# Performance work log

Measured on AMD Instinct MI355X. Metric: run time of the kernel, lower is better.

Reference implementation:

```python
import jax, jax.numpy as jnp
import numpy as np
import math

B, L, D = 2, 4096, 1024
H, DK, DV = 4, 256, 256
CHUNK = 32
PROB_FLOOR = 0.02


def _l2norm(x, eps=1e-6):
    return x * jax.lax.rsqrt(jnp.sum(x * x, -1, keepdims=True) + eps)


def _silu(x):
    return x * jax.nn.sigmoid(x)


def _short_conv(x, w):
    # x: (b, l, c); w: (c, K). Depthwise causal conv + SiLU (ShortConvolution).
    K = w.shape[-1]
    xp = jnp.pad(x, ((0, 0), (K - 1, 0), (0, 0)))
    y = sum(xp[:, j:j + x.shape[1], :] * w[:, j] for j in range(K))
    return _silu(y)


def _fir_conv(x, filt):
    # x: (b, l, h, d); filt: (h, d, K). Depthwise causal FIR, no activation.
    b, l, h, d = x.shape
    K = filt.shape[-1]
    xf = jnp.pad(x.reshape(b, l, h * d).transpose(0, 2, 1), ((0, 0), (0, 0), (K - 1, 0)))
    w = filt.reshape(h * d, 1, K)
    y = jax.lax.conv_general_dilated(xf, w, (1,), 'VALID',
                                     dimension_numbers=('NCH', 'OIH', 'NCH'),
                                     feature_group_count=h * d)
    return y.transpose(0, 2, 1).reshape(b, l, h, d)


def _delta_rule_chunkwise(q, k, v, beta, chunk=CHUNK):
    # q,k: (b,h,L,dk); v: (b,h,L,dv); beta: (b,h,L). L % chunk == 0.
    b, h, Lq, dk = q.shape
    dv = v.shape[-1]
    n = Lq // chunk
    q = _l2norm(q)
    k = _l2norm(k)
    v = v * beta[..., None]
    kb = k * beta[..., None]
    rs = lambda t: t.reshape(b, h, n, chunk, t.shape[-1])
    qc, kc, vc, kbc = rs(q), rs(k), rs(v), rs(kb)
    strict_lower = jnp.tril(jnp.ones((chunk, chunk), bool), -1)
    # M = strictly-lower part of k_beta @ k^T; the in-place row recursion in the
    # torch code computes (I + M)^{-1} (unit lower-triangular inverse).
    M = jnp.where(strict_lower, jnp.einsum('bhncd,bhnmd->bhncm', kbc, kc), 0.0)
    eye = jnp.eye(chunk, dtype=q.dtype)
    T = jax.scipy.linalg.solve_triangular(eye + M, jnp.broadcast_to(eye, M.shape),
                                          lower=True, unit_diagonal=True)
    u = T @ vc       # (b,h,n,c,dv)
    w = T @ kbc      # (b,h,n,c,dk)
    incl_lower = jnp.tril(jnp.ones((chunk, chunk), bool), 0)

    def step(S, xs):
        q_i, k_i, u_i, w_i = xs  # (b,h,c,d)
        attn = jnp.where(incl_lower, q_i @ k_i.swapaxes(-1, -2), 0.0)
        u_adj = u_i - w_i @ S
        out_i = q_i @ S + attn @ u_adj
        S = S + k_i.swapaxes(-1, -2) @ u_adj
        return S, out_i

    S0 = jnp.zeros((b, h, dk, dv), q.dtype)
    xs = tuple(jnp.moveaxis(t, 2, 0) for t in (qc, kc, u, w))
    S, out = jax.lax.scan(step, S0, xs)
    out = jnp.moveaxis(out, 0, 2).reshape(b, h, Lq, dv)
    return out, S


def _rmsnorm(x, w, eps=1e-5):
    return x * jax.lax.rsqrt(jnp.mean(x * x, -1, keepdims=True) + eps) * w


def _per_head_stats(x):
    mean = jnp.mean(x, -1, keepdims=True)
    var = jnp.var(x, -1, keepdims=True)
    am = jnp.mean(jnp.abs(x), -1, keepdims=True)
    l2 = jnp.sqrt(jnp.sum(x * x, -1, keepdims=True))
    return jnp.concatenate([mean, var, am, l2], -1)  # (...,4)


def setup_inputs() -> dict:
    key = jax.random.key(0)
    ks = jax.random.split(key, 16)
    s = 0.02
    hidden_gate = D * 2 // 2  # fusion_hidden_mult=2 -> 1024
    gate_in_dim = D + 16
    inp = {
        'hidden_states': jax.random.normal(ks[0], (B, L, D), jnp.float32),
        'q_w': jax.random.normal(ks[1], (D, D), jnp.float32) * s,
        'k_w': jax.random.normal(ks[2], (D, D), jnp.float32) * s,
        'v_w': jax.random.normal(ks[3], (D, D), jnp.float32) * s,
        'b_w': jax.random.normal(ks[4], (H, D), jnp.float32) * s,
        'q_cw': jax.random.normal(ks[5], (D, 4), jnp.float32) * s,
        'k_cw': jax.random.normal(ks[6], (D, 4), jnp.float32) * s,
        'v_cw': jax.random.normal(ks[7], (D, 4), jnp.float32) * s,
        'fir_short_w': jax.random.normal(ks[8], (H, DV, 5), jnp.float32) * s,
        'fir_long_w': jax.random.normal(ks[9], (H, DV, 64), jnp.float32) * s,
        'mlp1_w': jax.random.normal(ks[10], (hidden_gate, gate_in_dim), jnp.float32) * s,
        'mlp1_b': jnp.zeros((hidden_gate,), jnp.float32),
        'mlp2_w': jax.random.normal(ks[11], (4, hidden_gate), jnp.float32) * s,
        'mlp2_b': jnp.array([-0.5, -0.5, 1.0, 3.0], jnp.float32),
        'logit_temp': jnp.full((1,), math.log(math.expm1(0.7)), jnp.float32),
        'conv_res_logit': jnp.full((H,), -2.0, jnp.float32),
        'norm_w': jnp.ones((DV,), jnp.float32),
        'o_w': jax.random.normal(ks[12], (D, D), jnp.float32) * s,
    }
    return inp


def _forward(hidden_states, q_w, k_w, v_w, b_w, q_cw, k_cw, v_cw,
             fir_short_w, fir_long_w, mlp1_w, mlp1_b, mlp2_w, mlp2_b,
             logit_temp, conv_res_logit, norm_w, o_w):
    b, l, _ = hidden_states.shape
    # projections + short causal depthwise convs (SiLU, qk_activation='silu')
    q_in = _short_conv(hidden_states @ q_w.T, q_cw)
    k_in = _short_conv(hidden_states @ k_w.T, k_cw)
    v_in = _short_conv(hidden_states @ v_w.T, v_cw)
    q = q_in.reshape(b, l, H, DK)
    k = k_in.reshape(b, l, H, DK)
    v_direct = v_in.reshape(b, l, H, DV)
    # qk_activation='silu' handled in conv; qk_norm='l2' handled inside delta rule
    beta = jnp.maximum(jax.nn.sigmoid(hidden_states @ b_w.T), 1e-6)  # (b,l,H)
    delta_out, _S = _delta_rule_chunkwise(
        q.transpose(0, 2, 1, 3), k.transpose(0, 2, 1, 3),
        v_direct.transpose(0, 2, 1, 3), beta.transpose(0, 2, 1))
    delta_out = delta_out.transpose(0, 2, 1, 3)  # (b,l,H,DV)
    local_short = _fir_conv(v_direct, fir_short_w)
    local_long = _fir_conv(v_direct, fir_long_w)
    stats = jnp.concatenate([_per_head_stats(local_short), _per_head_stats(local_long),
                             _per_head_stats(delta_out), _per_head_stats(v_direct)], -1)  # (b,l,H,16)
    hs_exp = jnp.broadcast_to(hidden_states[:, :, None, :], (b, l, H, hidden_states.shape[-1]))
    gate_in = jnp.concatenate([hs_exp, stats], -1)  # (b,l,H,D+16)
    h1 = jax.nn.gelu(gate_in @ mlp1_w.T + mlp1_b)
    logits = h1 @ mlp2_w.T + mlp2_b  # (b,l,H,4)
    temp = jax.nn.softplus(logit_temp)
    p = jax.nn.softmax(logits / temp, -1)
    p = jnp.maximum(p, PROB_FLOOR)
    p = p / jnp.sum(p, -1, keepdims=True)
    o = (p[..., 0:1] * local_short + p[..., 1:2] * local_long +
         p[..., 2:3] * delta_out + p[..., 3:4] * v_direct)
    # balanced residual conv injection (per-head learned static gate)
    o = o + jax.nn.sigmoid(conv_res_logit)[None, None, :, None] * local_short
    o = _rmsnorm(o, norm_w)
    o = o.reshape(b, l, H * DV) @ o_w.T
    return o


def reference(hidden_states, q_w, k_w, v_w, b_w, q_cw, k_cw, v_cw,
              fir_short_w, fir_long_w, mlp1_w, mlp1_b, mlp2_w, mlp2_b,
              logit_temp, conv_res_logit, norm_w, o_w):
    return _forward(hidden_states, q_w, k_w, v_w, b_w, q_cw, k_cw, v_cw,
                    fir_short_w, fir_long_w, mlp1_w, mlp1_b, mlp2_w, mlp2_b,
                    logit_temp, conv_res_logit, norm_w, o_w)
```

## Files before the change

### kernel.cpp

```cpp
#include <hip/hip_runtime.h>
#include <hip/hip_bf16.h>
#include <math.h>

#define NB 2
#define NL 4096
#define ND 1024
#define NH 4
#define NDK 256
#define NDV 256
#define NCH 128
#define NBL (NB*NL)

typedef __attribute__((ext_vector_type(8))) short short8;
typedef __attribute__((ext_vector_type(4))) short short4v;
typedef __attribute__((ext_vector_type(4))) float float4v;

#define MFMA16(a,b,c) __builtin_amdgcn_mfma_f32_16x16x32_bf16(a,b,c,0,0,0)

__device__ __forceinline__ short f2bs(float f){
  union { __hip_bfloat16 h; short s; } u; u.h = __float2bfloat16(f); return u.s;
}
__device__ __forceinline__ float bs2f(short s){
  union { float f; unsigned u; } u; u.u = ((unsigned)(unsigned short)s) << 16; return u.f;
}
__device__ __forceinline__ void store_c(float* p, float v){ *p = v; }
__device__ __forceinline__ void store_c(short* p, float v){ *p = f2bs(v); }

__device__ __forceinline__ void gload16(const short* g, short* l){
  __builtin_amdgcn_global_load_lds(
      (const __attribute__((address_space(1))) unsigned int*)g,
      (__attribute__((address_space(3))) unsigned int*)l, 16, 0, 0);
}
__device__ __forceinline__ void lds_barrier(){
  asm volatile("s_waitcnt lgkmcnt(0)" ::: "memory");
  __builtin_amdgcn_s_barrier();
  asm volatile("" ::: "memory");
}

__global__ void k_cast8(const float* __restrict__ s, short* __restrict__ d, int n8){
  int i = blockIdx.x*256 + threadIdx.x;
  if(i >= n8) return;
  const float4v a = *(const float4v*)(s + (size_t)i*8);
  const float4v b = *(const float4v*)(s + (size_t)i*8 + 4);
  short8 o;
  #pragma unroll
  for(int j=0;j<4;j++){ o[j] = f2bs(a[j]); o[4+j] = f2bs(b[j]); }
  *(short8*)(d + (size_t)i*8) = o;
}
__global__ void k_cast_w1a(const float* __restrict__ s, short* __restrict__ d){
  int i = blockIdx.x*256 + threadIdx.x;
  int r = i >> 7, c0 = (i & 127)*8;
  const float* sp = s + (size_t)r*1040 + c0;
  const float4v a = *(const float4v*)sp;
  const float4v b = *(const float4v*)(sp + 4);
  short8 o;
  #pragma unroll
  for(int j=0;j<4;j++){ o[j] = f2bs(a[j]); o[4+j] = f2bs(b[j]); }
  *(short8*)(d + (size_t)r*1024 + c0) = o;
}

__launch_bounds__(256)
__global__ void k_gemm4(const short* __restrict__ A, const short* __restrict__ Bt,
                        short* __restrict__ oq, short* __restrict__ ok,
                        short* __restrict__ ov, short* __restrict__ og){
  const int K = 1024;
  __shared__ short As[128*32];
  __shared__ short Bs[128*32];
  const int tid = threadIdx.x;
  const int w = tid >> 6, lane = tid & 63, lr = lane & 15, lg = lane >> 4;
  const int bm = blockIdx.x*128 + (w >> 1)*64;
  const int bnl = (blockIdx.y & 7)*128 + (w & 1)*64;
  short* C = (blockIdx.y>>3)==0 ? oq : (blockIdx.y>>3)==1 ? ok
           : (blockIdx.y>>3)==2 ? ov : og;
  float4v acc[4][4];
  #pragma unroll
  for(int i=0;i<4;i++)
    #pragma unroll
    for(int j=0;j<4;j++) acc[i][j] = (float4v){0.f,0.f,0.f,0.f};
  const short* ga0 = A  + (size_t)(blockIdx.x*128 + (tid>>2))*K + (tid&3)*8;
  const short* ga1 = ga0 + (size_t)64*K;
  const short* gb0 = Bt + (size_t)(blockIdx.y*128 + (tid>>2))*K + (tid&3)*8;
  const short* gb1 = gb0 + (size_t)64*K;
  short* la0 = As + w*512;
  short* la1 = As + 2048 + w*512;
  short* lb0 = Bs + w*512;
  short* lb1 = Bs + 2048 + w*512;
  const int arow = (w>>1)*64, brow = (w&1)*64;
  for(int kk=0; kk<K; kk+=32){
    gload16(ga0+kk, la0);
    gload16(ga1+kk, la1);
    gload16(gb0+kk, lb0);
    gload16(gb1+kk, lb1);
    __syncthreads();
    short8 a[4], b[4];
    #pragma unroll
    for(int i=0;i<4;i++) a[i] = *(const short8*)(As + (arow + i*16 + lr)*32 + lg*8);
    #pragma unroll
    for(int j=0;j<4;j++) b[j] = *(const short8*)(Bs + (brow + j*16 + lr)*32 + lg*8);
    #pragma unroll
    for(int i=0;i<4;i++)
      #pragma unroll
      for(int j=0;j<4;j++)
        acc[i][j] = MFMA16(a[i], b[j], acc[i][j]);
    __syncthreads();
  }
  #pragma unroll
  for(int i=0;i<4;i++){
    int row0 = bm + i*16 + lg*4;
    #pragma unroll
    for(int j=0;j<4;j++){
      short* cp = C + (size_t)row0*1024 + bnl + j*16 + lr;
      #pragma unroll
      for(int r=0;r<4;r++) cp[(size_t)r*1024] = f2bs(acc[i][j][r]);
    }
  }
}

template<typename OT>
__launch_bounds__(256)
__global__ void k_gemm(const short* __restrict__ A, const short* __restrict__ Bt,
                       OT* __restrict__ C, int M, int N, int K){
  __shared__ short As[128*32];
  __shared__ short Bs[128*32];
  const int tid = threadIdx.x;
  const int w = tid >> 6, lane = tid & 63, lr = lane & 15, lg = lane >> 4;
  const int bm = blockIdx.x*128 + (w >> 1)*64;
  const int bn = blockIdx.y*128 + (w & 1)*64;
  float4v acc[4][4];
  #pragma unroll
  for(int i=0;i<4;i++)
    #pragma unroll
    for(int j=0;j<4;j++) acc[i][j] = (float4v){0.f,0.f,0.f,0.f};
  const short* ga0 = A  + (size_t)(blockIdx.x*128 + (tid>>2))*K + (tid&3)*8;
  const short* ga1 = ga0 + (size_t)64*K;
  const short* gb0 = Bt + (size_t)(blockIdx.y*128 + (tid>>2))*K + (tid&3)*8;
  const short* gb1 = gb0 + (size_t)64*K;
  short* la0 = As + w*512;
  short* la1 = As + 2048 + w*512;
  short* lb0 = Bs + w*512;
  short* lb1 = Bs + 2048 + w*512;
  const int arow = (w>>1)*64, brow = (w&1)*64;
  for(int kk=0; kk<K; kk+=32){
    gload16(ga0+kk, la0);
    gload16(ga1+kk, la1);
    gload16(gb0+kk, lb0);
    gload16(gb1+kk, lb1);
    __syncthreads();
    short8 a[4], b[4];
    #pragma unroll
    for(int i=0;i<4;i++) a[i] = *(const short8*)(As + (arow + i*16 + lr)*32 + lg*8);
    #pragma unroll
    for(int j=0;j<4;j++) b[j] = *(const short8*)(Bs + (brow + j*16 + lr)*32 + lg*8);
    #pragma unroll
    for(int i=0;i<4;i++)
      #pragma unroll
      for(int j=0;j<4;j++)
        acc[i][j] = MFMA16(a[i], b[j], acc[i][j]);
    __syncthreads();
  }
  #pragma unroll
  for(int i=0;i<4;i++){
    int row0 = bm + i*16 + lg*4;
    #pragma unroll
    for(int j=0;j<4;j++){
      OT* cp = C + (size_t)row0*N + bn + j*16 + lr;
      #pragma unroll
      for(int r=0;r<4;r++) store_c(cp + (size_t)r*N, acc[i][j][r]);
    }
  }
}

__global__ void k_conv_silu(const short* __restrict__ x, const float* __restrict__ wgt,
                            short* __restrict__ y){
  int i8 = blockIdx.x*256 + threadIdx.x;
  int c0 = (i8 & 127)*8;
  int l = (i8 >> 7) & (NL-1);
  size_t base = (size_t)i8*8;
  short8 xv[4];
  #pragma unroll
  for(int t=0;t<4;t++)
    xv[t] = (l >= t) ? *(const short8*)(x + base - (size_t)t*1024)
                     : (short8){0,0,0,0,0,0,0,0};
  short8 o;
  #pragma unroll
  for(int j=0;j<8;j++){
    const float4v w4 = *(const float4v*)(wgt + (c0+j)*4);
    float acc = 0.f;
    #pragma unroll
    for(int t=0;t<4;t++) if(l >= t) acc += bs2f(xv[t][j]) * w4[3-t];
    o[j] = f2bs(acc / (1.f + __expf(-acc)));
  }
  *(short8*)(y + base) = o;
}

__global__ void k_beta(const float* __restrict__ hs, const float* __restrict__ bw,
                       float* __restrict__ beta){
  int w = threadIdx.x >> 6, lane = threadIdx.x & 63;
  int bl = blockIdx.x*4 + w;
  const float* x = hs + (size_t)bl*1024;
  float a[4] = {0.f,0.f,0.f,0.f};
  for(int d=lane; d<1024; d+=64){
    float xv = x[d];
    #pragma unroll
    for(int hh=0;hh<4;hh++) a[hh] += xv * bw[hh*1024 + d];
  }
  #pragma unroll
  for(int off=32; off; off>>=1)
    #pragma unroll
    for(int hh=0;hh<4;hh++) a[hh] += __shfl_down(a[hh], off);
  if(lane == 0)
    #pragma unroll
    for(int hh=0;hh<4;hh++)
      beta[(size_t)bl*4 + hh] = fmaxf(1.f/(1.f+__expf(-a[hh])), 1e-6f);
}

#define PADA 260
__launch_bounds__(256)
__global__ void k_phaseA(const short* __restrict__ q, const short* __restrict__ k,
                         const short* __restrict__ v, const float* __restrict__ beta,
                         short* __restrict__ qn_o, short* __restrict__ wn_o,
                         short* __restrict__ kT_o, short* __restrict__ at_o,
                         float* __restrict__ u_o){
  __shared__ float qn[32*PADA];
  __shared__ float kn[32*PADA];
  __shared__ float vb[32*PADA];
  __shared__ float kb[32*PADA];
  __shared__ float Ml[32*33];
  __shared__ float bet[32];
  const int tid = threadIdx.x;
  const int n = blockIdx.x % NCH;
  const int h = (blockIdx.x / NCH) % NH;
  const int b = blockIdx.x / (NCH*NH);
  size_t rowbase = ((size_t)b*NL + n*32)*1024 + h*256;
  if(tid < 32) bet[tid] = beta[((size_t)b*NL + n*32 + tid)*4 + h];
  for(int r=0;r<32;r++){
    qn[r*PADA + tid] = bs2f(q[rowbase + (size_t)r*1024 + tid]);
    kn[r*PADA + tid] = bs2f(k[rowbase + (size_t)r*1024 + tid]);
    vb[r*PADA + tid] = bs2f(v[rowbase + (size_t)r*1024 + tid]);
  }
  __syncthreads();
  {
    int row = tid >> 3, sub = tid & 7;
    float sq = 0.f, sk = 0.f;
    for(int kk=0; kk<32; kk++){
      int d = sub + 8*kk;
      float a0 = qn[row*PADA+d]; sq += a0*a0;
      float a1 = kn[row*PADA+d]; sk += a1*a1;
    }
    #pragma unroll
    for(int off=1; off<8; off<<=1){ sq += __shfl_xor(sq, off); sk += __shfl_xor(sk, off); }
    float rq = rsqrtf(sq + 1e-6f), rk = rsqrtf(sk + 1e-6f);
    float be = bet[row];
    for(int kk=0; kk<32; kk++){
      int d = sub + 8*kk;
      qn[row*PADA+d] *= rq;
      float kv = kn[row*PADA+d]*rk;
      kn[row*PADA+d] = kv;
      kb[row*PADA+d] = kv*be;
      vb[row*PADA+d] *= be;
    }
  }
  __syncthreads();
  {
    int w = tid >> 6, lane = tid & 63, lr = lane & 15, lg = lane >> 4;
    int m0 = (w & 1)*16;
    const float* Asrc = (w < 2) ? kb : qn;
    float4v acc0 = (float4v){0.f,0.f,0.f,0.f}, acc1 = (float4v){0.f,0.f,0.f,0.f};
    for(int kc=0; kc<8; kc++){
      int kof = kc*32 + lg*8;
      short8 af, b0, b1;
      const float* ap  = Asrc + (m0+lr)*PADA + kof;
      const float* bp0 = kn + lr*PADA + kof;
      const float* bp1 = kn + (16+lr)*PADA + kof;
      #pragma unroll
      for(int j=0;j<8;j++){ af[j]=f2bs(ap[j]); b0[j]=f2bs(bp0[j]); b1[j]=f2bs(bp1[j]); }
      acc0 = MFMA16(af, b0, acc0);
      acc1 = MFMA16(af, b1, acc1);
    }
    if(w < 2){
      #pragma unroll
      for(int r=0;r<4;r++){
        int row = m0 + lg*4 + r;
        Ml[row*33 + lr]      = (lr      < row) ? acc0[r] : 0.f;
        Ml[row*33 + 16 + lr] = ((16+lr) < row) ? acc1[r] : 0.f;
      }
    } else {
      size_t abase = (size_t)blockIdx.x * 1024;
      #pragma unroll
      for(int r=0;r<4;r++){
        int row = m0 + lg*4 + r;
        at_o[abase + row*32 + lr]      = (lr      <= row) ? f2bs(acc0[r]) : (short)0;
        at_o[abase + row*32 + 16 + lr] = ((16+lr) <= row) ? f2bs(acc1[r]) : (short)0;
      }
    }
  }
  __syncthreads();
  {
    int d = tid;
    for(int i=1;i<32;i++){
      float su = 0.f, sw = 0.f;
      const float* Mr = Ml + i*33;
      for(int t=0;t<i;t++){
        float m = Mr[t];
        su += m * vb[t*PADA + d];
        sw += m * kb[t*PADA + d];
      }
      vb[i*PADA + d] -= su;
      kb[i*PADA + d] -= sw;
    }
  }
  __syncthreads();
  {
    size_t obase = (size_t)blockIdx.x * 8192;
    for(int it=0; it<32; it++){
      int idx = it*256 + tid;
      qn_o[obase + idx] = f2bs(qn[it*PADA + tid]);
      wn_o[obase + idx] = f2bs(-kb[it*PADA + tid]);
      u_o [obase + idx] = vb[it*PADA + tid];
      int tt = idx & 31, dd = idx >> 5;
      kT_o[obase + idx] = f2bs(kn[tt*PADA + dd]);
    }
  }
}

struct FragsB {
  short8 a[8];
  short8 kt[4];
  short8 at;
  float4v u;
};

__device__ __forceinline__ void loadFrags(FragsB& f, size_t cb,
    const short* __restrict__ qn, const short* __restrict__ wn,
    const short* __restrict__ kT, const short* __restrict__ at,
    const float* __restrict__ u, int w, int lr, int lg, int m0, int c0){
  const short* kT_b = kT + cb*8192;
  #pragma unroll
  for(int mi=0;mi<4;mi++)
    f.kt[mi] = *(const short8*)(kT_b + ((w*4+mi)*16 + lr)*32 + lg*8);
  if(w < 2){
    const short* wn_b = wn + cb*8192;
    #pragma unroll
    for(int kc=0;kc<8;kc++)
      f.a[kc] = *(const short8*)(wn_b + (m0+lr)*256 + kc*32 + lg*8);
    const float* up = u + cb*8192 + (size_t)(m0 + lg*4)*256 + c0 + lr;
    #pragma unroll
    for(int r=0;r<4;r++) f.u[r] = up[(size_t)r*256];
  } else {
    const short* qn_b = qn + cb*8192;
    #pragma unroll
    for(int kc=0;kc<8;kc++)
      f.a[kc] = *(const short8*)(qn_b + (m0+lr)*256 + kc*32 + lg*8);
    f.at = *(const short8*)(at + cb*1024 + (m0+lr)*32 + lg*8);
  }
}

__device__ __forceinline__ void computeChunk(const FragsB& f, int n,
    float4v (&Sreg)[4], float* __restrict__ ua, short* __restrict__ ScT,
    short* __restrict__ dout, int b, int h, int c0,
    int w, int lr, int lg, int m0, int swz){
  char* scb = (char*)ScT;
  lds_barrier();
  float4v oacc = (float4v){0.f,0.f,0.f,0.f};
  if(w < 2){
    float4v acc = f.u, acc2 = (float4v){0.f,0.f,0.f,0.f};
    #pragma unroll
    for(int kc=0;kc<4;kc++){
      short8 s0 = *(const short8*)(scb + (((lr<<9) + ((kc*32 + lg*8)<<1)) ^ swz));
      short8 s1 = *(const short8*)(scb + (((lr<<9) + (((kc+4)*32 + lg*8)<<1)) ^ swz));
      acc  = MFMA16(f.a[kc],   s0, acc);
      acc2 = MFMA16(f.a[kc+4], s1, acc2);
    }
    #pragma unroll
    for(int r=0;r<4;r++) ua[(m0 + lg*4 + r)*18 + lr] = acc[r] + acc2[r];
  } else {
    float4v acc2 = (float4v){0.f,0.f,0.f,0.f};
    #pragma unroll
    for(int kc=0;kc<4;kc++){
      short8 s0 = *(const short8*)(scb + (((lr<<9) + ((kc*32 + lg*8)<<1)) ^ swz));
      short8 s1 = *(const short8*)(scb + (((lr<<9) + (((kc+4)*32 + lg*8)<<1)) ^ swz));
      oacc = MFMA16(f.a[kc],   s0, oacc);
      acc2 = MFMA16(f.a[kc+4], s1, acc2);
    }
    #pragma unroll
    for(int r=0;r<4;r++) oacc[r] += acc2[r];
  }
  lds_barrier();
  short8 bu;
  #pragma unroll
  for(int j=0;j<8;j++) bu[j] = f2bs(ua[(lg*8 + j)*18 + lr]);
  if(w >= 2){
    oacc = MFMA16(f.at, bu, oacc);
    short* ob = dout + ((size_t)b*NL + n*32 + m0 + lg*4)*1024 + h*256 + c0 + lr;
    #pragma unroll
    for(int r=0;r<4;r++) ob[(size_t)r*1024] = f2bs(oacc[r]);
  }
  #pragma unroll
  for(int mi=0; mi<4; mi++){
    Sreg[mi] = MFMA16(f.kt[mi], bu, Sreg[mi]);
    int rowb = (w*4 + mi)*16 + lg*4;
    short4v pk;
    #pragma unroll
    for(int r=0;r<4;r++) pk[r] = f2bs(Sreg[mi][r]);
    *(short4v*)(scb + (((lr<<9) + (rowb<<1)) ^ swz)) = pk;
  }
}

__launch_bounds__(256, 1)
__global__ void k_phaseB(const short* __restrict__ qn, const short* __restrict__ wn,
                         const short* __restrict__ kT, const short* __restrict__ at,
                         const float* __restrict__ u, short* __restrict__ dout){
  __shared__ float ua[32*18];
  __shared__ short ScT[4096];
  const int tid = threadIdx.x;
  const int chain = blockIdx.x & 7;
  const int cblk = blockIdx.x >> 3;
  const int b = chain >> 2, h = chain & 3;
  const int c0 = cblk * 16;
  for(int i=tid; i<4096; i+=256) ScT[i] = 0;
  const int w = tid >> 6, lane = tid & 63, lr = lane & 15, lg = lane >> 4;
  const int m0 = (w & 1)*16;
  const size_t chunkbase = (size_t)(b*NH + h) * NCH;
  const int swz = (lr & 7) << 4;
  float4v Sreg[4];
  #pragma unroll
  for(int mi=0;mi<4;mi++) Sreg[mi] = (float4v){0.f,0.f,0.f,0.f};
  __syncthreads();
  FragsB fA, fB;
  loadFrags(fA, chunkbase, qn, wn, kT, at, u, w, lr, lg, m0, c0);
  for(int n=0; n<NCH; n+=2){
    loadFrags(fB, chunkbase + n+1, qn, wn, kT, at, u, w, lr, lg, m0, c0);
    computeChunk(fA, n, Sreg, ua, ScT, dout, b, h, c0, w, lr, lg, m0, swz);
    if(n+2 < NCH)
      loadFrags(fA, chunkbase + n+2, qn, wn, kT, at, u, w, lr, lg, m0, c0);
    computeChunk(fB, n+1, Sreg, ua, ScT, dout, b, h, c0, w, lr, lg, m0, swz);
  }
}

__launch_bounds__(256, 2)
__global__ void k_fir(const short* __restrict__ v, const float* __restrict__ wS,
                      const float* __restrict__ wL, short* __restrict__ ls,
                      short* __restrict__ ll){
  const int tid = threadIdx.x;
  const int lt = blockIdx.x % (NL/32);
  const int h = (blockIdx.x / (NL/32)) % NH;
  const int b = blockIdx.x / ((NL/32)*NH);
  const int l0 = lt*32;
  const size_t colbase = (size_t)b*NL*1024 + h*256 + tid;
  const float* wLp = wL + (size_t)h*16384 + tid*64;
  const float* wSp = wS + (size_t)h*1280 + tid*5;
  float accL[32], accS[32];
  #pragma unroll
  for(int i=0;i<32;i++){ accL[i]=0.f; accS[i]=0.f; }
  {
    float w[32];
    #pragma unroll
    for(int j=0;j<32;j++) w[j] = wLp[j];
    float val[63];
    #pragma unroll
    for(int s=0;s<63;s++){
      int l = l0 - 63 + s;
      int lc = l < 0 ? 0 : l;
      float x = bs2f(v[colbase + (size_t)lc*1024]);
      val[s] = l < 0 ? 0.f : x;
    }
    #pragma unroll
    for(int i=0;i<32;i++)
      #pragma unroll
      for(int j=0;j<32;j++)
        accL[i] += val[i+j]*w[j];
  }
  {
    float w[32];
    #pragma unroll
    for(int j=0;j<32;j++) w[j] = wLp[32+j];
    float w5[5];
    #pragma unroll
    for(int j=0;j<5;j++) w5[j] = wSp[j];
    float val[63];
    #pragma unroll
    for(int s=0;s<63;s++){
      int l = l0 - 31 + s;
      int lc = l < 0 ? 0 : l;
      float x = bs2f(v[colbase + (size_t)lc*1024]);
      val[s] = l < 0 ? 0.f : x;
    }
    #pragma unroll
    for(int i=0;i<32;i++){
      #pragma unroll
      for(int j=0;j<32;j++)
        accL[i] += val[i+j]*w[j];
      #pragma unroll
      for(int j=0;j<5;j++)
        accS[i] += val[i+27+j]*w5[j];
    }
  }
  #pragma unroll
  for(int i=0;i<32;i++){
    size_t ox = colbase + (size_t)(l0+i)*1024;
    ll[ox] = f2bs(accL[i]);
    ls[ox] = f2bs(accS[i]);
  }
}

__launch_bounds__(256)
__global__ void k_gatecomb(const short* __restrict__ ls, const short* __restrict__ ll,
                           const short* __restrict__ dd, const short* __restrict__ vv,
                           const short* __restrict__ G, const float* __restrict__ w1,
                           const float* __restrict__ b1, const float* __restrict__ w2,
                           const float* __restrict__ b2, const float* __restrict__ ltp,
                           const float* __restrict__ crl, const float* __restrict__ nw,
                           short* __restrict__ obf){
  __shared__ float st[4][16];
  __shared__ float red[4][4];
  __shared__ float pl[4][4];
  __shared__ float rr2[4][4];
  const int tid = threadIdx.x;
  const size_t bl = blockIdx.x;
  {
    int row = tid >> 4, ln = tid & 15;
    int ten = row >> 2, hh = row & 3;
    const short* base = (ten==0 ? ls : ten==1 ? ll : ten==2 ? dd : vv) + (bl*4 + hh)*256;
    float s1=0.f, s2=0.f, sa=0.f;
    for(int kk=0; kk<16; kk++){
      float x = bs2f(base[ln + 16*kk]);
      s1 += x; s2 += x*x; sa += fabsf(x);
    }
    #pragma unroll
    for(int off=1; off<16; off<<=1){
      s1 += __shfl_xor(s1, off); s2 += __shfl_xor(s2, off); sa += __shfl_xor(sa, off);
    }
    if(ln == 0){
      float mean = s1 * (1.f/256.f);
      st[hh][ten*4+0] = mean;
      st[hh][ten*4+1] = s2*(1.f/256.f) - mean*mean;
      st[hh][ten*4+2] = sa*(1.f/256.f);
      st[hh][ten*4+3] = sqrtf(s2);
    }
  }
  __syncthreads();
  const int w = tid >> 6, lane = tid & 63;
  float temp = log1pf(__expf(ltp[0]));
  for(int hh=0; hh<4; hh++){
    float sreg[16];
    #pragma unroll
    for(int s=0;s<16;s++) sreg[s] = st[hh][s];
    float lg4[4] = {0.f,0.f,0.f,0.f};
    for(int ii=0; ii<4; ii++){
      int i = tid + ii*256;
      float g = bs2f(G[bl*1024 + i]) + b1[i];
      const float* wr = w1 + (size_t)i*1040 + 1024;
      #pragma unroll
      for(int s=0;s<16;s++) g += sreg[s]*wr[s];
      float z = 1.5957691216057308f*(g + 0.044715f*g*g*g);
      float hg = g / (1.f + __expf(-z));
      #pragma unroll
      for(int jj=0;jj<4;jj++) lg4[jj] += hg * w2[jj*1024 + i];
    }
    #pragma unroll
    for(int off=32; off; off>>=1)
      #pragma unroll
      for(int jj=0;jj<4;jj++) lg4[jj] += __shfl_down(lg4[jj], off);
    if(lane == 0)
      #pragma unroll
      for(int jj=0;jj<4;jj++) red[w][jj] = lg4[jj];
    __syncthreads();
    if(tid == 0){
      float lo[4]; float mx = -1e30f;
      #pragma unroll
      for(int jj=0;jj<4;jj++){
        lo[jj] = (red[0][jj]+red[1][jj]+red[2][jj]+red[3][jj] + b2[jj]) / temp;
        mx = fmaxf(mx, lo[jj]);
      }
      float e[4], se = 0.f;
      #pragma unroll
      for(int jj=0;jj<4;jj++){ e[jj] = __expf(lo[jj]-mx); se += e[jj]; }
      float s2 = 0.f;
      #pragma unroll
      for(int jj=0;jj<4;jj++){ e[jj] = fmaxf(e[jj]/se, 0.02f); s2 += e[jj]; }
      float inv = 1.f/s2;
      #pragma unroll
      for(int jj=0;jj<4;jj++) pl[hh][jj] = e[jj]*inv;
    }
    __syncthreads();
  }
  float o4[4], ss4[4];
  #pragma unroll
  for(int h=0; h<4; h++){
    size_t ix = (bl*4 + h)*256 + tid;
    float rg = 1.f/(1.f + __expf(-crl[h]));
    float o = (pl[h][0] + rg)*bs2f(ls[ix]) + pl[h][1]*bs2f(ll[ix])
            + pl[h][2]*bs2f(dd[ix]) + pl[h][3]*bs2f(vv[ix]);
    o4[h] = o;
    ss4[h] = o*o;
  }
  #pragma unroll
  for(int off=32; off; off>>=1)
    #pragma unroll
    for(int h=0; h<4; h++) ss4[h] += __shfl_down(ss4[h], off);
  if(lane == 0)
    #pragma unroll
    for(int h=0; h<4; h++) rr2[w][h] = ss4[h];
  __syncthreads();
  float nwv = nw[tid];
  #pragma unroll
  for(int h=0; h<4; h++){
    float tot = rr2[0][h]+rr2[1][h]+rr2[2][h]+rr2[3][h];
    float rms = rsqrtf(tot*(1.f/256.f) + 1e-5f);
    size_t ix = (bl*4 + h)*256 + tid;
    obf[ix] = f2bs(o4[h]*rms*nwv);
  }
}

extern "C" void kernel_launch(void* const* d_in, const int* in_sizes, int n_in,
                              void* d_out, int out_size, void* d_ws, size_t ws_size,
                              hipStream_t stream){
  const float* hs  = (const float*)d_in[0];
  const float* qw  = (const float*)d_in[1];
  const float* kw  = (const float*)d_in[2];
  const float* vw  = (const float*)d_in[3];
  const float* bw  = (const float*)d_in[4];
  const float* qcw = (const float*)d_in[5];
  const float* kcw = (const float*)d_in[6];
  const float* vcw = (const float*)d_in[7];
  const float* fsw = (const float*)d_in[8];
  const float* flw = (const float*)d_in[9];
  const float* w1  = (const float*)d_in[10];
  const float* b1  = (const float*)d_in[11];
  const float* w2  = (const float*)d_in[12];
  const float* b2  = (const float*)d_in[13];
  const float* ltp = (const float*)d_in[14];
  const float* crl = (const float*)d_in[15];
  const float* nw  = (const float*)d_in[16];
  const float* ow  = (const float*)d_in[17];

  char* ws = (char*)d_ws;
  size_t off = 0;
  auto alloc = [&](size_t bytes)->char*{
    char* pp = ws + off; off += (bytes + 255) & ~(size_t)255; return pp;
  };
  short* hs_bf  = (short*)alloc((size_t)NBL*1024*2);
  short* wmega  = (short*)alloc((size_t)4096*1024*2);
  short* qp_bf  = (short*)alloc((size_t)NBL*1024*2);
  short* kp_bf  = (short*)alloc((size_t)NBL*1024*2);
  short* vp_bf  = (short*)alloc((size_t)NBL*1024*2);
  short* g_bf   = (short*)alloc((size_t)NBL*1024*2);
  short* qc_bf  = (short*)alloc((size_t)NBL*1024*2);
  short* kc_bf  = (short*)alloc((size_t)NBL*1024*2);
  short* vc_bf  = (short*)alloc((size_t)NBL*1024*2);
  float* u_f    = (float*)alloc((size_t)NBL*1024*4);
  short* do_bf  = (short*)alloc((size_t)NBL*1024*2);
  short* at_bf  = (short*)alloc((size_t)NB*NH*NCH*1024*2);
  float* beta   = (float*)alloc((size_t)NBL*4*4);
  if(ws_size < off) return;

  short* qn_bf = qp_bf; short* wn_bf = kp_bf; short* kT_bf = vp_bf;
  short* ls_bf = qc_bf; short* ll_bf = kc_bf;
  short* o_bf  = kp_bf;

  k_cast8<<<dim3(4096),dim3(256),0,stream>>>(hs, hs_bf, NBL*1024/8);
  k_cast8<<<dim3(512),dim3(256),0,stream>>>(qw, wmega, 1024*1024/8);
  k_cast8<<<dim3(512),dim3(256),0,stream>>>(kw, wmega + 1024*1024, 1024*1024/8);
  k_cast8<<<dim3(512),dim3(256),0,stream>>>(vw, wmega + 2*1024*1024, 1024*1024/8);
  k_cast_w1a<<<dim3(512),dim3(256),0,stream>>>(w1, wmega + 3*1024*1024);
  k_gemm4<<<dim3(64,32),dim3(256),0,stream>>>(hs_bf, wmega, qp_bf, kp_bf, vp_bf, g_bf);
  k_conv_silu<<<dim3(4096),dim3(256),0,stream>>>(qp_bf, qcw, qc_bf);
  k_conv_silu<<<dim3(4096),dim3(256),0,stream>>>(kp_bf, kcw, kc_bf);
  k_conv_silu<<<dim3(4096),dim3(256),0,stream>>>(vp_bf, vcw, vc_bf);
  k_beta<<<dim3(2048),dim3(256),0,stream>>>(hs, bw, beta);
  k_phaseA<<<dim3(1024),dim3(256),0,stream>>>(qc_bf, kc_bf, vc_bf, beta,
                                              qn_bf, wn_bf, kT_bf, at_bf, u_f);
  k_phaseB<<<dim3(128),dim3(256),0,stream>>>(qn_bf, wn_bf, kT_bf, at_bf, u_f, do_bf);
  k_fir<<<dim3(1024),dim3(256),0,stream>>>(vc_bf, fsw, flw, ls_bf, ll_bf);
  k_gatecomb<<<dim3(8192),dim3(256),0,stream>>>(ls_bf, ll_bf, do_bf, vc_bf, g_bf,
                                                w1, b1, w2, b2, ltp, crl, nw, o_bf);
  k_cast8<<<dim3(512),dim3(256),0,stream>>>(ow, wmega, 1024*1024/8);
  k_gemm<float><<<dim3(64,8),dim3(256),0,stream>>>(o_bf, wmega, (float*)d_out,
                                                   NBL, 1024, 1024);
}
```

Measured before the change: 587.6 us.

## Collapse delta-rule recurrence kernel to single wavefront per block, removing barriers

The sequential chunk recurrence kernel now runs with one 64-lane wavefront per block instead of four. That one wave holds the whole 256x16 state slice in registers and computes the u-correction, the output and the state update itself. LDS exchanges are kept only within the wave, so the per-chunk workgroup barriers and the cross-wave staging are gone. The explicit double-buffered fragment prefetch is dropped, and each chunk's loads are issued inline. The trade-off is that each serial step now does four times more work per wave, with less memory-level parallelism and no explicit prefetch.

After: 1.464 ms. 149% more time.

```diff
diff --git a/kernel.cpp b/kernel.cpp
--- a/kernel.cpp
+++ b/kernel.cpp
@@ -30,11 +30,6 @@
   __builtin_amdgcn_global_load_lds(
       (const __attribute__((address_space(1))) unsigned int*)g,
       (__attribute__((address_space(3))) unsigned int*)l, 16, 0, 0);
-}
-__device__ __forceinline__ void lds_barrier(){
-  asm volatile("s_waitcnt lgkmcnt(0)" ::: "memory");
-  __builtin_amdgcn_s_barrier();
-  asm volatile("" ::: "memory");
 }
 
 __global__ void k_cast8(const float* __restrict__ s, short* __restrict__ d, int n8){
@@ -323,117 +318,90 @@
   }
 }
 
-struct FragsB {
-  short8 a[8];
-  short8 kt[4];
-  short8 at;
-  float4v u;
-};
-
-__device__ __forceinline__ void loadFrags(FragsB& f, size_t cb,
-    const short* __restrict__ qn, const short* __restrict__ wn,
-    const short* __restrict__ kT, const short* __restrict__ at,
-    const float* __restrict__ u, int w, int lr, int lg, int m0, int c0){
-  const short* kT_b = kT + cb*8192;
-  #pragma unroll
-  for(int mi=0;mi<4;mi++)
-    f.kt[mi] = *(const short8*)(kT_b + ((w*4+mi)*16 + lr)*32 + lg*8);
-  if(w < 2){
-    const short* wn_b = wn + cb*8192;
-    #pragma unroll
-    for(int kc=0;kc<8;kc++)
-      f.a[kc] = *(const short8*)(wn_b + (m0+lr)*256 + kc*32 + lg*8);
-    const float* up = u + cb*8192 + (size_t)(m0 + lg*4)*256 + c0 + lr;
-    #pragma unroll
-    for(int r=0;r<4;r++) f.u[r] = up[(size_t)r*256];
-  } else {
-    const short* qn_b = qn + cb*8192;
-    #pragma unroll
-    for(int kc=0;kc<8;kc++)
-      f.a[kc] = *(const short8*)(qn_b + (m0+lr)*256 + kc*32 + lg*8);
-    f.at = *(const short8*)(at + cb*1024 + (m0+lr)*32 + lg*8);
-  }
-}
-
-__device__ __forceinline__ void computeChunk(const FragsB& f, int n,
-    float4v (&Sreg)[4], float* __restrict__ ua, short* __restrict__ ScT,
-    short* __restrict__ dout, int b, int h, int c0,
-    int w, int lr, int lg, int m0, int swz){
-  char* scb = (char*)ScT;
-  lds_barrier();
-  float4v oacc = (float4v){0.f,0.f,0.f,0.f};
-  if(w < 2){
-    float4v acc = f.u, acc2 = (float4v){0.f,0.f,0.f,0.f};
-    #pragma unroll
-    for(int kc=0;kc<4;kc++){
-      short8 s0 = *(const short8*)(scb + (((lr<<9) + ((kc*32 + lg*8)<<1)) ^ swz));
-      short8 s1 = *(const short8*)(scb + (((lr<<9) + (((kc+4)*32 + lg*8)<<1)) ^ swz));
-      acc  = MFMA16(f.a[kc],   s0, acc);
-      acc2 = MFMA16(f.a[kc+4], s1, acc2);
-    }
-    #pragma unroll
-    for(int r=0;r<4;r++) ua[(m0 + lg*4 + r)*18 + lr] = acc[r] + acc2[r];
-  } else {
-    float4v acc2 = (float4v){0.f,0.f,0.f,0.f};
-    #pragma unroll
-    for(int kc=0;kc<4;kc++){
-      short8 s0 = *(const short8*)(scb + (((lr<<9) + ((kc*32 + lg*8)<<1)) ^ swz));
-      short8 s1 = *(const short8*)(scb + (((lr<<9) + (((kc+4)*32 + lg*8)<<1)) ^ swz));
-      oacc = MFMA16(f.a[kc],   s0, oacc);
-      acc2 = MFMA16(f.a[kc+4], s1, acc2);
-    }
-    #pragma unroll
-    for(int r=0;r<4;r++) oacc[r] += acc2[r];
-  }
-  lds_barrier();
-  short8 bu;
-  #pragma unroll
-  for(int j=0;j<8;j++) bu[j] = f2bs(ua[(lg*8 + j)*18 + lr]);
-  if(w >= 2){
-    oacc = MFMA16(f.at, bu, oacc);
-    short* ob = dout + ((size_t)b*NL + n*32 + m0 + lg*4)*1024 + h*256 + c0 + lr;
-    #pragma unroll
-    for(int r=0;r<4;r++) ob[(size_t)r*1024] = f2bs(oacc[r]);
-  }
-  #pragma unroll
-  for(int mi=0; mi<4; mi++){
-    Sreg[mi] = MFMA16(f.kt[mi], bu, Sreg[mi]);
-    int rowb = (w*4 + mi)*16 + lg*4;
-    short4v pk;
-    #pragma unroll
-    for(int r=0;r<4;r++) pk[r] = f2bs(Sreg[mi][r]);
-    *(short4v*)(scb + (((lr<<9) + (rowb<<1)) ^ swz)) = pk;
-  }
-}
-
-__launch_bounds__(256, 1)
+__launch_bounds__(64, 1)
 __global__ void k_phaseB(const short* __restrict__ qn, const short* __restrict__ wn,
                          const short* __restrict__ kT, const short* __restrict__ at,
                          const float* __restrict__ u, short* __restrict__ dout){
-  __shared__ float ua[32*18];
   __shared__ short ScT[4096];
+  __shared__ short uaT[512];
   const int tid = threadIdx.x;
+  const int lr = tid & 15, lg = tid >> 4;
   const int chain = blockIdx.x & 7;
   const int cblk = blockIdx.x >> 3;
   const int b = chain >> 2, h = chain & 3;
   const int c0 = cblk * 16;
-  for(int i=tid; i<4096; i+=256) ScT[i] = 0;
-  const int w = tid >> 6, lane = tid & 63, lr = lane & 15, lg = lane >> 4;
-  const int m0 = (w & 1)*16;
+  for(int i=tid; i<4096; i+=64) ScT[i] = 0;
   const size_t chunkbase = (size_t)(b*NH + h) * NCH;
+  char* scb = (char*)ScT;
+  char* uab = (char*)uaT;
   const int swz = (lr & 7) << 4;
-  float4v Sreg[4];
-  #pragma unroll
-  for(int mi=0;mi<4;mi++) Sreg[mi] = (float4v){0.f,0.f,0.f,0.f};
-  __syncthreads();
-  FragsB fA, fB;
-  loadFrags(fA, chunkbase, qn, wn, kT, at, u, w, lr, lg, m0, c0);
-  for(int n=0; n<NCH; n+=2){
-    loadFrags(fB, chunkbase + n+1, qn, wn, kT, at, u, w, lr, lg, m0, c0);
-    computeChunk(fA, n, Sreg, ua, ScT, dout, b, h, c0, w, lr, lg, m0, swz);
-    if(n+2 < NCH)
-      loadFrags(fA, chunkbase + n+2, qn, wn, kT, at, u, w, lr, lg, m0, c0);
-    computeChunk(fB, n+1, Sreg, ua, ScT, dout, b, h, c0, w, lr, lg, m0, swz);
+  const int uswz = (lr & 3) << 4;
+  float4v Sreg[16];
+  #pragma unroll
+  for(int t=0;t<16;t++) Sreg[t] = (float4v){0.f,0.f,0.f,0.f};
+  for(int n=0; n<NCH; n++){
+    size_t cb = chunkbase + n;
+    const short* qn_b = qn + cb*8192;
+    const short* wn_b = wn + cb*8192;
+    const short* kT_b = kT + cb*8192;
+    const short* at_b = at + cb*1024;
+    const float* u_b  = u + cb*8192 + c0;
+    short8 Sb[8];
+    #pragma unroll
+    for(int kc=0;kc<8;kc++)
+      Sb[kc] = *(const short8*)(scb + (((lr<<9) + ((kc*32+lg*8)<<1)) ^ swz));
+    float4v ua0, ua1;
+    {
+      const float* up = u_b + (size_t)lg*1024 + lr;
+      #pragma unroll
+      for(int r=0;r<4;r++){ ua0[r] = up[(size_t)r*256]; ua1[r] = up[4096 + (size_t)r*256]; }
+      #pragma unroll
+      for(int kc=0;kc<8;kc++){
+        short8 w0 = *(const short8*)(wn_b + lr*256 + kc*32 + lg*8);
+        short8 w1 = *(const short8*)(wn_b + (16+lr)*256 + kc*32 + lg*8);
+        ua0 = MFMA16(w0, Sb[kc], ua0);
+        ua1 = MFMA16(w1, Sb[kc], ua1);
+      }
+    }
+    {
+      short4v p0, p1;
+      #pragma unroll
+      for(int r=0;r<4;r++){ p0[r] = f2bs(ua0[r]); p1[r] = f2bs(ua1[r]); }
+      *(short4v*)(uab + (((lr<<6) + (lg<<3)) ^ uswz)) = p0;
+      *(short4v*)(uab + (((lr<<6) + 32 + (lg<<3)) ^ uswz)) = p1;
+    }
+    float4v o0 = (float4v){0.f,0.f,0.f,0.f}, o1 = (float4v){0.f,0.f,0.f,0.f};
+    #pragma unroll
+    for(int kc=0;kc<8;kc++){
+      short8 q0 = *(const short8*)(qn_b + lr*256 + kc*32 + lg*8);
+      short8 q1 = *(const short8*)(qn_b + (16+lr)*256 + kc*32 + lg*8);
+      o0 = MFMA16(q0, Sb[kc], o0);
+      o1 = MFMA16(q1, Sb[kc], o1);
+    }
+    short8 bu = *(const short8*)(uab + (((lr<<6) + (lg<<4)) ^ uswz));
+    {
+      short8 a0 = *(const short8*)(at_b + lr*32 + lg*8);
+      short8 a1 = *(const short8*)(at_b + (16+lr)*32 + lg*8);
+      o0 = MFMA16(a0, bu, o0);
+      o1 = MFMA16(a1, bu, o1);
+    }
+    {
+      short* ob = dout + ((size_t)b*NL + n*32 + lg*4)*1024 + h*256 + c0 + lr;
+      #pragma unroll
+      for(int r=0;r<4;r++){
+        ob[(size_t)r*1024] = f2bs(o0[r]);
+        ob[(size_t)(16 + r)*1024] = f2bs(o1[r]);
+      }
+    }
+    #pragma unroll
+    for(int mt=0;mt<16;mt++){
+      short8 kf = *(const short8*)(kT_b + (mt*16+lr)*32 + lg*8);
+      Sreg[mt] = MFMA16(kf, bu, Sreg[mt]);
+      short4v pk;
+      #pragma unroll
+      for(int r=0;r<4;r++) pk[r] = f2bs(Sreg[mt][r]);
+      *(short4v*)(scb + (((lr<<9) + ((mt*16+lg*4)<<1)) ^ swz)) = pk;
+    }
   }
 }
 
@@ -670,7 +638,7 @@
   k_beta<<<dim3(2048),dim3(256),0,stream>>>(hs, bw, beta);
   k_phaseA<<<dim3(1024),dim3(256),0,stream>>>(qc_bf, kc_bf, vc_bf, beta,
                                               qn_bf, wn_bf, kT_bf, at_bf, u_f);
-  k_phaseB<<<dim3(128),dim3(256),0,stream>>>(qn_bf, wn_bf, kT_bf, at_bf, u_f, do_bf);
+  k_phaseB<<<dim3(128),dim3(64),0,stream>>>(qn_bf, wn_bf, kT_bf, at_bf, u_f, do_bf);
   k_fir<<<dim3(1024),dim3(256),0,stream>>>(vc_bf, fsw, flw, ls_bf, ll_bf);
   k_gatecomb<<<dim3(8192),dim3(256),0,stream>>>(ls_bf, ll_bf, do_bf, vc_bf, g_bf,
                                                 w1, b1, w2, b2, ltp, crl, nw, o_bf);
```
